# Kernel tuning notes

Hardware: AMD Instinct MI355X
Metric: run time of the kernel (lower is better)

## Reference

```python
import jax, jax.numpy as jnp
import numpy as np

I = 512   # input_size
H = 512   # hidden_size
Z = 0.1   # zoneout rate (eval-mode deterministic blend)
S = 128   # number of segments
B = 64    # batch


def setup_inputs() -> dict:
    rng = np.random.default_rng(0)
    durs = rng.integers(4, 13, size=(S, B)).astype(np.int64)  # [S, B], all >= 1
    T = int(durs.sum(0).max())
    key = jax.random.key(0)
    k0, k1, k2, k3, k4 = jax.random.split(key, 5)
    k = 1.0 / np.sqrt(H)
    x = jax.random.normal(k0, (T, B, I), jnp.float32)
    W_ih = jax.random.uniform(k1, (4 * H, I), jnp.float32, -k, k)
    W_hh = jax.random.uniform(k2, (4 * H, H), jnp.float32, -k, k)
    b_ih = jax.random.uniform(k3, (4 * H,), jnp.float32, -k, k)
    b_hh = jax.random.uniform(k4, (4 * H,), jnp.float32, -k, k)
    return {"x": x, "durs": jnp.asarray(durs), "W_ih": W_ih, "W_hh": W_hh,
            "b_ih": b_ih, "b_hh": b_hh}


def _duration_masks(durs, T):
    # durs: [S, B] -> per-batch segment-end (reset) frame indices and masks
    durs_bs = durs.T                                   # [B, S]
    reset_idx = jnp.cumsum(durs_bs, axis=1) - 1        # [B, S] last frame of each segment
    mel_lengths = jnp.sum(durs_bs, axis=1)             # [B]
    t = jnp.arange(T)
    reset_mask = jnp.any(t[None, :, None] == reset_idx[:, None, :], axis=-1)  # [B, T]
    valid = t[None, :] < mel_lengths[:, None]          # [B, T] frames within mel length
    retain = (~reset_mask) & valid                     # state kept where not reset/pad
    return reset_idx, retain.T, valid.T                # retain/valid as [T, B]


def reference(x, durs, W_ih, W_hh, b_ih, b_hh):
    T, Bb, _ = x.shape
    reset_idx, retain, valid = _duration_masks(durs, T)
    # Precompute the input contribution to the gates for all timesteps (one big GEMM)
    xg = jnp.einsum('tbi,gi->tbg', x, W_ih) + b_ih + b_hh   # [T, B, 4H]
    retain_f = retain.astype(x.dtype)                       # [T, B]

    def step(carry, inp):
        h, c = carry
        xg_t, retain_t = inp
        gates = xg_t + h @ W_hh.T                           # [B, 4H]
        i, f, g, o = jnp.split(gates, 4, axis=-1)           # torch LSTMCell order i,f,g,o
        i = jax.nn.sigmoid(i); f = jax.nn.sigmoid(f); o = jax.nn.sigmoid(o)
        g = jnp.tanh(g)
        c_new = f * c + i * g
        h_new = o * jnp.tanh(c_new)
        # eval-mode zoneout: deterministic blend with previous state
        h_z = Z * h + (1.0 - Z) * h_new
        c_z = Z * c + (1.0 - Z) * c_new
        m = retain_t[:, None]                               # zero state at segment resets / padding
        return (h_z * m, c_z * m), h_z

    h0 = jnp.zeros((Bb, H), x.dtype)
    (h, c), outputs = jax.lax.scan(step, (h0, h0), (xg, retain_f))
    outputs = outputs * valid[:, :, None].astype(outputs.dtype)  # [T, B, H]
    # segout: hidden state at each segment's last frame -> [B, S, H]
    segout = jnp.take_along_axis(outputs.transpose(1, 0, 2), reset_idx[:, :, None], axis=1)
    return outputs, h, c, segout
```

## Files before the change

### kernel.cpp

```cpp
#include <hip/hip_runtime.h>
#include <hip/hip_fp16.h>

#define IDIM 512
#define HDIM 512
#define NGATE 2048
#define SEGS 128
#define BATCH 64
#define ZK 0.1f

typedef _Float16 f16;
typedef _Float16 f16x8 __attribute__((ext_vector_type(8)));
typedef float f32x4 __attribute__((ext_vector_type(4)));

__device__ __forceinline__ void gload16(const void* g, void* l) {
  __builtin_amdgcn_global_load_lds((const __attribute__((address_space(1))) void*)g,
                                   (__attribute__((address_space(3))) void*)l, 16, 0, 0);
}
__device__ __forceinline__ float sigmoidf_(float x) { return 1.0f / (1.0f + __expf(-x)); }
__device__ __forceinline__ float tanhf_(float x) { return 2.0f / (1.0f + __expf(-2.0f * x)) - 1.0f; }

__global__ void prep_kernel(const int* __restrict__ durs, int4* __restrict__ meta,
                            int* __restrict__ Mk, int* __restrict__ mel) {
  __shared__ int hist[16];
  __shared__ int cur[16];
  int tid = threadIdx.x;
  if (tid < 16) hist[tid] = 0;
  __syncthreads();
  int b = tid;
  for (int s = 0; s < SEGS; ++s) atomicAdd(&hist[durs[s * BATCH + b] & 15], 1);
  __syncthreads();
  if (tid == 0) {
    int run = 0;
    for (int d = 15; d >= 0; --d) { cur[d] = run; run += hist[d]; }
    for (int kk = 0; kk < 12; ++kk) Mk[kk] = cur[kk];
  }
  __syncthreads();
  int run = 0;
  for (int s = 0; s < SEGS; ++s) {
    int d = durs[s * BATCH + b] & 15;
    int pos = atomicAdd(&cur[d], 1);
    meta[pos] = make_int4(run, b, s, d);
    run += d;
  }
  mel[b] = run;
}

__global__ void wprep_kernel(const float* __restrict__ Wih, const float* __restrict__ Whh,
                             const float* __restrict__ bih, const float* __restrict__ bhh,
                             f16* __restrict__ Wc, float* __restrict__ biasp) {
  int n = blockIdx.x;
  int G = n >> 6, q = (n >> 4) & 3, r = n & 15;
  int j = G * 16 + r;
  int orig = q * 512 + j;
  for (int kk = threadIdx.x; kk < 1024; kk += blockDim.x) {
    float v = (kk < 512) ? Wih[(size_t)orig * 512 + kk] : Whh[(size_t)orig * 512 + kk - 512];
    Wc[(size_t)n * 1024 + kk] = (f16)v;
  }
  if (threadIdx.x == 0) biasp[n] = bih[orig] + bhh[orig];
}

__global__ void xconv_kernel(const float* __restrict__ x, f16* __restrict__ xh, long n8) {
  long i = (long)blockIdx.x * blockDim.x + threadIdx.x;
  long stride = (long)gridDim.x * blockDim.x;
  for (; i < n8; i += stride) {
    const float4* p = (const float4*)(x + i * 8);
    float4 a = p[0], bv = p[1];
    f16x8 o;
    o[0] = (f16)a.x;  o[1] = (f16)a.y;  o[2] = (f16)a.z;  o[3] = (f16)a.w;
    o[4] = (f16)bv.x; o[5] = (f16)bv.y; o[6] = (f16)bv.z; o[7] = (f16)bv.w;
    *(f16x8*)(xh + i * 8) = o;
  }
}

__global__ void zero_kernel(float* __restrict__ out, const int* __restrict__ mel,
                            int T, int total) {
  int tb = T * BATCH;
  for (int bid = blockIdx.x; bid < total; bid += gridDim.x) {
    if (bid < tb) {
      int t = bid / BATCH, b = bid - t * BATCH;
      if (t < mel[b]) continue;
      float4* p = (float4*)(out + (size_t)bid * HDIM);
      p[threadIdx.x] = make_float4(0.f, 0.f, 0.f, 0.f);
    } else {
      int e = bid - tb;
      float4* p = (float4*)(out + (size_t)tb * HDIM + (size_t)e * HDIM);
      p[threadIdx.x] = make_float4(0.f, 0.f, 0.f, 0.f);
    }
  }
}

template <bool FIRST>
__global__ __launch_bounds__(512, 1)
void step256_kernel(const f16* __restrict__ xh, const f16* __restrict__ Wc,
                    const float* __restrict__ biasp,
                    const f16* __restrict__ hprev, f16* __restrict__ hnext,
                    float* __restrict__ cst,
                    const int4* __restrict__ meta, const int* __restrict__ Mk,
                    float* __restrict__ out, int T, int k) {
  const int mk = Mk[k];
  const int id = blockIdx.y * 8 + blockIdx.x;
  const int xcd = id & 7, slot = id >> 3;
  const int by = (slot & 3) * 8 + xcd;
  const int bx = slot >> 2;
  const int m0 = by * 256;
  if (m0 >= mk) return;
  const int n0 = bx * 256;

  __shared__ __align__(16) f16 As[2][256][64];
  __shared__ __align__(16) f16 Bs[2][256][64];
  __shared__ int4 metaS[256];

  const int tid = threadIdx.x;
  const int lane = tid & 63;
  const int w = tid >> 6;
  const int wr = w >> 2;
  const int wc = w & 3;
  const int lr = lane & 15;
  const int lk = lane >> 4;

  if (tid < 256) metaS[tid] = meta[m0 + tid];

  const int swzc = (((lane & 7) ^ ((lane >> 3) & 7)) << 3);
  size_t xoff[4];
  int ra4[4];
#pragma unroll
  for (int o = 0; o < 4; ++o) {
    int trow = o * 64 + w * 8 + (lane >> 3);
    int r = m0 + trow;
    int ra = (r < mk) ? r : 0;
    int4 mt = meta[ra];
    xoff[o] = ((size_t)(mt.x + k) * BATCH + mt.y) * IDIM + swzc;
    ra4[o] = ra;
  }

  auto stageA = [&](int o, int kb, int slot2) {
    const f16* src;
    if (FIRST || kb < 8) src = xh + xoff[o] + kb * 64;
    else src = hprev + (size_t)ra4[o] * HDIM + (kb - 8) * 64 + swzc;
    gload16(src, &As[slot2][o * 64 + w * 8][0]);
  };
  auto stageB = [&](int o, int kb, int slot2) {
    int trow = o * 64 + w * 8 + (lane >> 3);
    gload16(Wc + (size_t)(n0 + trow) * 1024 + (size_t)kb * 64 + swzc,
            &Bs[slot2][o * 64 + w * 8][0]);
  };

  auto lda = [&](int slot2, int h, int f, int ks) -> f16x8 {
    int row = wr * 128 + h * 64 + f * 16 + lr;
    int ch = (((ks * 4 + lk) ^ (lr & 7)) << 3);
    return *(const f16x8*)&As[slot2][row][ch];
  };
  auto ldb = [&](int slot2, int q, int ks) -> f16x8 {
    int row = wc * 64 + q * 16 + lr;
    int ch = (((ks * 4 + lk) ^ (lr & 7)) << 3);
    return *(const f16x8*)&Bs[slot2][row][ch];
  };

  f32x4 acc[8][4];
#pragma unroll
  for (int a = 0; a < 8; ++a)
#pragma unroll
    for (int bb = 0; bb < 4; ++bb) acc[a][bb] = (f32x4){0.f, 0.f, 0.f, 0.f};

  const int KB = FIRST ? 8 : 16;

#pragma unroll
  for (int o = 0; o < 4; ++o) stageA(o, 0, 0);
#pragma unroll
  for (int o = 0; o < 4; ++o) stageB(o, 0, 0);
#pragma unroll
  for (int o = 0; o < 4; ++o) stageA(o, 1, 1);
#pragma unroll
  for (int o = 0; o < 4; ++o) stageB(o, 1, 1);
  asm volatile("s_waitcnt vmcnt(8)" ::: "memory");
  __builtin_amdgcn_s_barrier();

  f16x8 aF[4][2], bF[4][2];

  for (int kt = 0; kt < KB; ++kt) {
    const int s = kt & 1;
    const bool st1 = (kt + 1 < KB);
    const bool st2 = (kt + 2 < KB);

#pragma unroll
    for (int f = 0; f < 4; ++f)
#pragma unroll
      for (int ks = 0; ks < 2; ++ks) aF[f][ks] = lda(s, 0, f, ks);
#pragma unroll
    for (int q = 0; q < 4; ++q)
#pragma unroll
      for (int ks = 0; ks < 2; ++ks) bF[q][ks] = ldb(s, q, ks);
    __builtin_amdgcn_s_barrier();
    __builtin_amdgcn_s_setprio(1);
#pragma unroll
    for (int f = 0; f < 4; ++f)
#pragma unroll
      for (int fn = 0; fn < 2; ++fn)
#pragma unroll
        for (int ks = 0; ks < 2; ++ks)
          acc[f][fn] = __builtin_amdgcn_mfma_f32_16x16x32_f16(aF[f][ks], bF[fn][ks], acc[f][fn], 0, 0, 0);
    __builtin_amdgcn_s_setprio(0);
    __builtin_amdgcn_s_barrier();

    if (st2) {
#pragma unroll
      for (int o = 0; o < 4; ++o) stageB(o, kt + 2, s);
    }
    __builtin_amdgcn_s_barrier();
    __builtin_amdgcn_s_setprio(1);
#pragma unroll
    for (int f = 0; f < 4; ++f)
#pragma unroll
      for (int fn = 2; fn < 4; ++fn)
#pragma unroll
        for (int ks = 0; ks < 2; ++ks)
          acc[f][fn] = __builtin_amdgcn_mfma_f32_16x16x32_f16(aF[f][ks], bF[fn][ks], acc[f][fn], 0, 0, 0);
    __builtin_amdgcn_s_setprio(0);
    __builtin_amdgcn_s_barrier();

#pragma unroll
    for (int f = 0; f < 4; ++f)
#pragma unroll
      for (int ks = 0; ks < 2; ++ks) aF[f][ks] = lda(s, 1, f, ks);
    if (st2) { stageA(0, kt + 2, s); stageA(2, kt + 2, s); }
    __builtin_amdgcn_s_barrier();
    __builtin_amdgcn_s_setprio(1);
#pragma unroll
    for (int f = 0; f < 4; ++f)
#pragma unroll
      for (int fn = 0; fn < 2; ++fn)
#pragma unroll
        for (int ks = 0; ks < 2; ++ks)
          acc[4 + f][fn] = __builtin_amdgcn_mfma_f32_16x16x32_f16(aF[f][ks], bF[fn][ks], acc[4 + f][fn], 0, 0, 0);
    __builtin_amdgcn_s_setprio(0);
    __builtin_amdgcn_s_barrier();

    if (st2) { stageA(1, kt + 2, s); stageA(3, kt + 2, s); }
    __builtin_amdgcn_s_setprio(1);
#pragma unroll
    for (int f = 0; f < 4; ++f)
#pragma unroll
      for (int fn = 2; fn < 4; ++fn)
#pragma unroll
        for (int ks = 0; ks < 2; ++ks)
          acc[4 + f][fn] = __builtin_amdgcn_mfma_f32_16x16x32_f16(aF[f][ks], bF[fn][ks], acc[4 + f][fn], 0, 0, 0);
    __builtin_amdgcn_s_setprio(0);
    if (st2) {
      asm volatile("s_waitcnt vmcnt(8)" ::: "memory");
    } else if (st1) {
      asm volatile("s_waitcnt vmcnt(0)" ::: "memory");
    }
    __builtin_amdgcn_s_barrier();
  }

  float bq[4];
#pragma unroll
  for (int q = 0; q < 4; ++q) bq[q] = biasp[n0 + wc * 64 + q * 16 + lr];
  const int j = ((n0 + wc * 64) >> 6) * 16 + lr;
  const size_t segoff = (size_t)T * BATCH * HDIM + (size_t)2 * BATCH * HDIM;

#pragma unroll
  for (int fm = 0; fm < 8; ++fm) {
#pragma unroll
    for (int reg = 0; reg < 4; ++reg) {
      int m = m0 + wr * 128 + fm * 16 + ((lane >> 4) << 2) + reg;
      if (m >= mk) continue;
      int4 mt = metaS[m - m0];
      float gi = acc[fm][0][reg] + bq[0];
      float gf = acc[fm][1][reg] + bq[1];
      float gg = acc[fm][2][reg] + bq[2];
      float go = acc[fm][3][reg] + bq[3];
      float iv = sigmoidf_(gi), fv = sigmoidf_(gf);
      float gv = tanhf_(gg), ov = sigmoidf_(go);
      float cp, hp;
      if (FIRST) { cp = 0.f; hp = 0.f; }
      else {
        cp = cst[(size_t)m * HDIM + j];
        hp = (float)hprev[(size_t)m * HDIM + j];
      }
      float cn = fv * cp + iv * gv;
      float hn = ov * tanhf_(cn);
      float hz = ZK * hp + (1.f - ZK) * hn;
      float cz = ZK * cp + (1.f - ZK) * cn;
      out[((size_t)(mt.x + k) * BATCH + mt.y) * HDIM + j] = hz;
      if (k == mt.w - 1) {
        out[segoff + ((size_t)mt.y * SEGS + mt.z) * HDIM + j] = hz;
      } else {
        hnext[(size_t)m * HDIM + j] = (f16)hz;
        cst[(size_t)m * HDIM + j] = cz;
      }
    }
  }
}

template <bool FIRST>
__global__ void step_kernel(const f16* __restrict__ xh, const f16* __restrict__ Wc,
                            const float* __restrict__ biasp,
                            const f16* __restrict__ hprev, f16* __restrict__ hnext,
                            float* __restrict__ cst,
                            const int4* __restrict__ meta, const int* __restrict__ Mk,
                            float* __restrict__ out, int T, int k) {
  const int mk = Mk[k];
  const int id = blockIdx.y * 16 + blockIdx.x;
  const int xcd = id & 7, slot = id >> 3;
  const int by = (slot & 7) * 8 + xcd;
  const int bx = slot >> 3;
  const int m0 = by * 128;
  if (m0 >= mk) return;
  const int n0 = bx * 128;

  __shared__ __align__(16) f16 At[128][64];
  __shared__ __align__(16) f16 Bt[128][64];
  __shared__ int4 metaS[128];

  const int tid = threadIdx.x;
  const int lane = tid & 63;
  const int w = tid >> 6;
  const int wr = w >> 1, wc = w & 1;

  if (tid < 128) metaS[tid] = meta[m0 + tid];

  const f16* xsrc[4];
  const f16* hsrc[4];
  const f16* wsrc[4];
#pragma unroll
  for (int i = 0; i < 4; ++i) {
    int r = m0 + w * 32 + i * 8 + (lane >> 3);
    int ra = (r < mk) ? r : 0;
    int4 mt = meta[ra];
    xsrc[i] = xh + ((size_t)(mt.x + k) * BATCH + mt.y) * IDIM;
    hsrc[i] = hprev + (size_t)ra * HDIM;
    wsrc[i] = Wc + (size_t)(n0 + w * 32 + i * 8 + (lane >> 3)) * 1024;
  }
  const int koff = (lane & 7) * 8;

  f32x4 acc[4][4];
#pragma unroll
  for (int a = 0; a < 4; ++a)
#pragma unroll
    for (int bb = 0; bb < 4; ++bb) acc[a][bb] = (f32x4){0.f, 0.f, 0.f, 0.f};

  const int KB = FIRST ? 8 : 16;
  for (int kb = 0; kb < KB; ++kb) {
    __syncthreads();
#pragma unroll
    for (int i = 0; i < 4; ++i) {
      const f16* s;
      if (FIRST) s = xsrc[i] + kb * 64 + koff;
      else       s = (kb < 8) ? (xsrc[i] + kb * 64 + koff) : (hsrc[i] + (kb - 8) * 64 + koff);
      gload16(s, &At[w * 32 + i * 8][0]);
    }
#pragma unroll
    for (int i = 0; i < 4; ++i) gload16(wsrc[i] + kb * 64 + koff, &Bt[w * 32 + i * 8][0]);
    __syncthreads();

    const int lr = lane & 15;
    const int lk = (lane >> 4) * 8;
#pragma unroll
    for (int ks = 0; ks < 2; ++ks) {
      f16x8 af[4], bfr[4];
#pragma unroll
      for (int f = 0; f < 4; ++f) af[f] = *(const f16x8*)&At[wr * 64 + f * 16 + lr][ks * 32 + lk];
#pragma unroll
      for (int f = 0; f < 4; ++f) bfr[f] = *(const f16x8*)&Bt[wc * 64 + f * 16 + lr][ks * 32 + lk];
#pragma unroll
      for (int fm = 0; fm < 4; ++fm)
#pragma unroll
        for (int fn = 0; fn < 4; ++fn)
          acc[fm][fn] = __builtin_amdgcn_mfma_f32_16x16x32_f16(af[fm], bfr[fn], acc[fm][fn], 0, 0, 0);
    }
  }

  const int r15 = lane & 15;
  float bq[4];
#pragma unroll
  for (int q = 0; q < 4; ++q) bq[q] = biasp[n0 + wc * 64 + q * 16 + r15];
  const int j = ((n0 + wc * 64) >> 6) * 16 + r15;
  const size_t segoff = (size_t)T * BATCH * HDIM + (size_t)2 * BATCH * HDIM;

#pragma unroll
  for (int fm = 0; fm < 4; ++fm) {
#pragma unroll
    for (int reg = 0; reg < 4; ++reg) {
      int m = m0 + wr * 64 + fm * 16 + ((lane >> 4) << 2) + reg;
      if (m >= mk) continue;
      int4 mt = metaS[m - m0];
      float gi = acc[fm][0][reg] + bq[0];
      float gf = acc[fm][1][reg] + bq[1];
      float gg = acc[fm][2][reg] + bq[2];
      float go = acc[fm][3][reg] + bq[3];
      float iv = sigmoidf_(gi), fv = sigmoidf_(gf);
      float gv = tanhf_(gg), ov = sigmoidf_(go);
      float cp, hp;
      if (FIRST) { cp = 0.f; hp = 0.f; }
      else {
        cp = cst[(size_t)m * HDIM + j];
        hp = (float)hprev[(size_t)m * HDIM + j];
      }
      float cn = fv * cp + iv * gv;
      float hn = ov * tanhf_(cn);
      float hz = ZK * hp + (1.f - ZK) * hn;
      float cz = ZK * cp + (1.f - ZK) * cn;
      out[((size_t)(mt.x + k) * BATCH + mt.y) * HDIM + j] = hz;
      if (k == mt.w - 1) {
        out[segoff + ((size_t)mt.y * SEGS + mt.z) * HDIM + j] = hz;
      } else {
        hnext[(size_t)m * HDIM + j] = (f16)hz;
        cst[(size_t)m * HDIM + j] = cz;
      }
    }
  }
}

extern "C" void kernel_launch(void* const* d_in, const int* in_sizes, int n_in,
                              void* d_out, int out_size, void* d_ws, size_t ws_size,
                              hipStream_t stream) {
  const float* x = (const float*)d_in[0];
  const int* durs = (const int*)d_in[1];
  const float* Wih = (const float*)d_in[2];
  const float* Whh = (const float*)d_in[3];
  const float* bih = (const float*)d_in[4];
  const float* bhh = (const float*)d_in[5];
  float* out = (float*)d_out;
  const int T = in_sizes[0] / (BATCH * IDIM);

  char* ws = (char*)d_ws;
  size_t off = 0;
  auto alloc = [&](size_t bytes) {
    void* p = ws + off;
    off = (off + bytes + 255) & ~(size_t)255;
    return p;
  };
  f16* xh     = (f16*)alloc((size_t)T * BATCH * IDIM * 2);
  f16* Wc     = (f16*)alloc((size_t)NGATE * 1024 * 2);
  float* biasp= (float*)alloc((size_t)NGATE * 4);
  f16* hst0   = (f16*)alloc((size_t)SEGS * BATCH * HDIM * 2);
  f16* hst1   = (f16*)alloc((size_t)SEGS * BATCH * HDIM * 2);
  float* cst  = (float*)alloc((size_t)SEGS * BATCH * HDIM * 4);
  int4* meta  = (int4*)alloc((size_t)SEGS * BATCH * 16);
  int* Mk     = (int*)alloc(64);
  int* mel    = (int*)alloc(64);

  prep_kernel<<<1, 64, 0, stream>>>(durs, meta, Mk, mel);
  wprep_kernel<<<NGATE, 256, 0, stream>>>(Wih, Whh, bih, bhh, Wc, biasp);
  long n8 = (long)T * BATCH * IDIM / 8;
  xconv_kernel<<<2048, 256, 0, stream>>>(x, xh, n8);
  zero_kernel<<<2048, 128, 0, stream>>>(out, mel, T, T * BATCH + 128);

  dim3 hgrid(8, 32);
  step256_kernel<true><<<hgrid, 512, 0, stream>>>(xh, Wc, biasp, hst0, hst1, cst, meta, Mk, out, T, 0);
  for (int k = 1; k < 8; ++k) {
    f16* hp = (k & 1) ? hst1 : hst0;
    f16* hn = (k & 1) ? hst0 : hst1;
    step256_kernel<false><<<hgrid, 512, 0, stream>>>(xh, Wc, biasp, hp, hn, cst, meta, Mk, out, T, k);
  }
  dim3 sgrid(16, 64);
  for (int k = 8; k < 12; ++k) {
    f16* hp = (k & 1) ? hst1 : hst0;
    f16* hn = (k & 1) ? hst0 : hst1;
    step_kernel<false><<<sgrid, 256, 0, stream>>>(xh, Wc, biasp, hp, hn, cst, meta, Mk, out, T, k);
  }
}
```

Before: 725.7 us.

## Rework 256x256 step GEMM to 4 waves with 128x128 per-wave tiles

The large-tile step kernel drops from 8 waves (512 threads) to 4 waves (256 threads), and each wave now computes a 128x128 output tile with a 64-entry accumulator array instead of 128x64. The k-loop is simplified to two MFMA phases per k-tile with fewer barriers, and all next-tile loads are issued in one group. The block-to-tile mapping swizzle is changed, and the smaller step kernel loses its XCD-aware remap in favour of direct blockIdx mapping. Larger per-wave tiles improve fragment reuse and cut barrier overhead, but they raise register pressure and leave fewer waves to hide latency.

```diff
diff --git a/kernel.cpp b/kernel.cpp
--- a/kernel.cpp
+++ b/kernel.cpp
@@ -90,7 +90,7 @@
 }
 
 template <bool FIRST>
-__global__ __launch_bounds__(512, 1)
+__global__ __launch_bounds__(256, 1)
 void step256_kernel(const f16* __restrict__ xh, const f16* __restrict__ Wc,
                     const float* __restrict__ biasp,
                     const f16* __restrict__ hprev, f16* __restrict__ hnext,
@@ -99,9 +99,8 @@
                     float* __restrict__ out, int T, int k) {
   const int mk = Mk[k];
   const int id = blockIdx.y * 8 + blockIdx.x;
-  const int xcd = id & 7, slot = id >> 3;
-  const int by = (slot & 3) * 8 + xcd;
-  const int bx = slot >> 2;
+  const int swz = (id & 7) * 32 + (id >> 3);
+  const int by = swz >> 3, bx = swz & 7;
   const int m0 = by * 256;
   if (m0 >= mk) return;
   const int n0 = bx * 256;
@@ -113,181 +112,163 @@
   const int tid = threadIdx.x;
   const int lane = tid & 63;
   const int w = tid >> 6;
-  const int wr = w >> 2;
-  const int wc = w & 3;
+  const int wr = w >> 1;
+  const int wc = w & 1;
   const int lr = lane & 15;
   const int lk = lane >> 4;
 
-  if (tid < 256) metaS[tid] = meta[m0 + tid];
+  metaS[tid] = meta[m0 + tid];
 
   const int swzc = (((lane & 7) ^ ((lane >> 3) & 7)) << 3);
-  size_t xoff[4];
-  int ra4[4];
-#pragma unroll
-  for (int o = 0; o < 4; ++o) {
-    int trow = o * 64 + w * 8 + (lane >> 3);
+  unsigned xoff[8];
+  int ra8[8];
+#pragma unroll
+  for (int o = 0; o < 8; ++o) {
+    int trow = o * 32 + w * 8 + (lane >> 3);
     int r = m0 + trow;
     int ra = (r < mk) ? r : 0;
     int4 mt = meta[ra];
-    xoff[o] = ((size_t)(mt.x + k) * BATCH + mt.y) * IDIM + swzc;
-    ra4[o] = ra;
-  }
-
-  auto stageA = [&](int o, int kb, int slot2) {
+    xoff[o] = (unsigned)(((mt.x + k) * BATCH + mt.y) * IDIM + swzc);
+    ra8[o] = ra;
+  }
+
+  auto stageA = [&](int o, int kb, int slot) {
     const f16* src;
-    if (FIRST || kb < 8) src = xh + xoff[o] + kb * 64;
-    else src = hprev + (size_t)ra4[o] * HDIM + (kb - 8) * 64 + swzc;
-    gload16(src, &As[slot2][o * 64 + w * 8][0]);
+    if (FIRST || kb < 8) src = xh + (size_t)xoff[o] + kb * 64;
+    else src = hprev + (size_t)ra8[o] * HDIM + (kb - 8) * 64 + swzc;
+    gload16(src, &As[slot][o * 32 + w * 8][0]);
   };
-  auto stageB = [&](int o, int kb, int slot2) {
-    int trow = o * 64 + w * 8 + (lane >> 3);
+  auto stageB = [&](int o, int kb, int slot) {
+    int trow = o * 32 + w * 8 + (lane >> 3);
     gload16(Wc + (size_t)(n0 + trow) * 1024 + (size_t)kb * 64 + swzc,
-            &Bs[slot2][o * 64 + w * 8][0]);
+            &Bs[slot][o * 32 + w * 8][0]);
   };
 
-  auto lda = [&](int slot2, int h, int f, int ks) -> f16x8 {
-    int row = wr * 128 + h * 64 + f * 16 + lr;
+  auto lda = [&](int slot, int mf, int ks) -> f16x8 {
+    int row = wr * 128 + mf * 16 + lr;
     int ch = (((ks * 4 + lk) ^ (lr & 7)) << 3);
-    return *(const f16x8*)&As[slot2][row][ch];
+    return *(const f16x8*)&As[slot][row][ch];
   };
-  auto ldb = [&](int slot2, int q, int ks) -> f16x8 {
-    int row = wc * 64 + q * 16 + lr;
+  auto ldb = [&](int slot, int nf, int ks) -> f16x8 {
+    int row = wc * 128 + nf * 16 + lr;
     int ch = (((ks * 4 + lk) ^ (lr & 7)) << 3);
-    return *(const f16x8*)&Bs[slot2][row][ch];
+    return *(const f16x8*)&Bs[slot][row][ch];
   };
 
-  f32x4 acc[8][4];
+  f32x4 acc[8][8];
 #pragma unroll
   for (int a = 0; a < 8; ++a)
 #pragma unroll
-    for (int bb = 0; bb < 4; ++bb) acc[a][bb] = (f32x4){0.f, 0.f, 0.f, 0.f};
+    for (int bb = 0; bb < 8; ++bb) acc[a][bb] = (f32x4){0.f, 0.f, 0.f, 0.f};
 
   const int KB = FIRST ? 8 : 16;
 
 #pragma unroll
-  for (int o = 0; o < 4; ++o) stageA(o, 0, 0);
-#pragma unroll
-  for (int o = 0; o < 4; ++o) stageB(o, 0, 0);
-#pragma unroll
-  for (int o = 0; o < 4; ++o) stageA(o, 1, 1);
-#pragma unroll
-  for (int o = 0; o < 4; ++o) stageB(o, 1, 1);
-  asm volatile("s_waitcnt vmcnt(8)" ::: "memory");
+  for (int o = 0; o < 8; ++o) { stageA(o, 0, 0); }
+#pragma unroll
+  for (int o = 0; o < 8; ++o) { stageB(o, 0, 0); }
+#pragma unroll
+  for (int o = 0; o < 8; ++o) { stageA(o, 1, 1); }
+#pragma unroll
+  for (int o = 0; o < 8; ++o) { stageB(o, 1, 1); }
+  asm volatile("s_waitcnt vmcnt(16)" ::: "memory");
   __builtin_amdgcn_s_barrier();
-
-  f16x8 aF[4][2], bF[4][2];
 
   for (int kt = 0; kt < KB; ++kt) {
     const int s = kt & 1;
     const bool st1 = (kt + 1 < KB);
     const bool st2 = (kt + 2 < KB);
 
-#pragma unroll
-    for (int f = 0; f < 4; ++f)
-#pragma unroll
-      for (int ks = 0; ks < 2; ++ks) aF[f][ks] = lda(s, 0, f, ks);
-#pragma unroll
-    for (int q = 0; q < 4; ++q)
-#pragma unroll
-      for (int ks = 0; ks < 2; ++ks) bF[q][ks] = ldb(s, q, ks);
+    f16x8 bF[8][2], aF0[8], aF1[8];
+#pragma unroll
+    for (int nf = 0; nf < 8; ++nf) {
+      bF[nf][0] = ldb(s, nf, 0);
+      bF[nf][1] = ldb(s, nf, 1);
+    }
+#pragma unroll
+    for (int mf = 0; mf < 8; ++mf) aF0[mf] = lda(s, mf, 0);
+
+    __builtin_amdgcn_s_setprio(1);
+#pragma unroll
+    for (int mf = 0; mf < 8; ++mf)
+#pragma unroll
+      for (int nf = 0; nf < 8; ++nf)
+        acc[mf][nf] = __builtin_amdgcn_mfma_f32_16x16x32_f16(aF0[mf], bF[nf][0], acc[mf][nf], 0, 0, 0);
+    __builtin_amdgcn_s_setprio(0);
+
+#pragma unroll
+    for (int mf = 0; mf < 8; ++mf) aF1[mf] = lda(s, mf, 1);
+
     __builtin_amdgcn_s_barrier();
+
+    if (st2) {
+#pragma unroll
+      for (int o = 0; o < 8; ++o) { stageA(o, kt + 2, s); }
+#pragma unroll
+      for (int o = 0; o < 8; ++o) { stageB(o, kt + 2, s); }
+    }
+
     __builtin_amdgcn_s_setprio(1);
 #pragma unroll
-    for (int f = 0; f < 4; ++f)
-#pragma unroll
-      for (int fn = 0; fn < 2; ++fn)
-#pragma unroll
-        for (int ks = 0; ks < 2; ++ks)
-          acc[f][fn] = __builtin_amdgcn_mfma_f32_16x16x32_f16(aF[f][ks], bF[fn][ks], acc[f][fn], 0, 0, 0);
+    for (int mf = 0; mf < 8; ++mf)
+#pragma unroll
+      for (int nf = 0; nf < 8; ++nf)
+        acc[mf][nf] = __builtin_amdgcn_mfma_f32_16x16x32_f16(aF1[mf], bF[nf][1], acc[mf][nf], 0, 0, 0);
     __builtin_amdgcn_s_setprio(0);
-    __builtin_amdgcn_s_barrier();
 
     if (st2) {
-#pragma unroll
-      for (int o = 0; o < 4; ++o) stageB(o, kt + 2, s);
-    }
-    __builtin_amdgcn_s_barrier();
-    __builtin_amdgcn_s_setprio(1);
-#pragma unroll
-    for (int f = 0; f < 4; ++f)
-#pragma unroll
-      for (int fn = 2; fn < 4; ++fn)
-#pragma unroll
-        for (int ks = 0; ks < 2; ++ks)
-          acc[f][fn] = __builtin_amdgcn_mfma_f32_16x16x32_f16(aF[f][ks], bF[fn][ks], acc[f][fn], 0, 0, 0);
-    __builtin_amdgcn_s_setprio(0);
-    __builtin_amdgcn_s_barrier();
-
-#pragma unroll
-    for (int f = 0; f < 4; ++f)
-#pragma unroll
-      for (int ks = 0; ks < 2; ++ks) aF[f][ks] = lda(s, 1, f, ks);
-    if (st2) { stageA(0, kt + 2, s); stageA(2, kt + 2, s); }
-    __builtin_amdgcn_s_barrier();
-    __builtin_amdgcn_s_setprio(1);
-#pragma unroll
-    for (int f = 0; f < 4; ++f)
-#pragma unroll
-      for (int fn = 0; fn < 2; ++fn)
-#pragma unroll
-        for (int ks = 0; ks < 2; ++ks)
-          acc[4 + f][fn] = __builtin_amdgcn_mfma_f32_16x16x32_f16(aF[f][ks], bF[fn][ks], acc[4 + f][fn], 0, 0, 0);
-    __builtin_amdgcn_s_setprio(0);
-    __builtin_amdgcn_s_barrier();
-
-    if (st2) { stageA(1, kt + 2, s); stageA(3, kt + 2, s); }
-    __builtin_amdgcn_s_setprio(1);
-#pragma unroll
-    for (int f = 0; f < 4; ++f)
-#pragma unroll
-      for (int fn = 2; fn < 4; ++fn)
-#pragma unroll
-        for (int ks = 0; ks < 2; ++ks)
-          acc[4 + f][fn] = __builtin_amdgcn_mfma_f32_16x16x32_f16(aF[f][ks], bF[fn][ks], acc[4 + f][fn], 0, 0, 0);
-    __builtin_amdgcn_s_setprio(0);
-    if (st2) {
-      asm volatile("s_waitcnt vmcnt(8)" ::: "memory");
+      asm volatile("s_waitcnt vmcnt(16)" ::: "memory");
     } else if (st1) {
       asm volatile("s_waitcnt vmcnt(0)" ::: "memory");
     }
     __builtin_amdgcn_s_barrier();
   }
 
-  float bq[4];
-#pragma unroll
-  for (int q = 0; q < 4; ++q) bq[q] = biasp[n0 + wc * 64 + q * 16 + lr];
-  const int j = ((n0 + wc * 64) >> 6) * 16 + lr;
+  float bq[2][4];
+#pragma unroll
+  for (int g2 = 0; g2 < 2; ++g2)
+#pragma unroll
+    for (int q = 0; q < 4; ++q)
+      bq[g2][q] = biasp[n0 + wc * 128 + g2 * 64 + q * 16 + lr];
+  int jg[2];
+#pragma unroll
+  for (int g2 = 0; g2 < 2; ++g2)
+    jg[g2] = ((n0 + wc * 128 + g2 * 64) >> 6) * 16 + lr;
   const size_t segoff = (size_t)T * BATCH * HDIM + (size_t)2 * BATCH * HDIM;
 
 #pragma unroll
-  for (int fm = 0; fm < 8; ++fm) {
+  for (int mf = 0; mf < 8; ++mf) {
 #pragma unroll
     for (int reg = 0; reg < 4; ++reg) {
-      int m = m0 + wr * 128 + fm * 16 + ((lane >> 4) << 2) + reg;
+      int m = m0 + wr * 128 + mf * 16 + ((lane >> 4) << 2) + reg;
       if (m >= mk) continue;
       int4 mt = metaS[m - m0];
-      float gi = acc[fm][0][reg] + bq[0];
-      float gf = acc[fm][1][reg] + bq[1];
-      float gg = acc[fm][2][reg] + bq[2];
-      float go = acc[fm][3][reg] + bq[3];
-      float iv = sigmoidf_(gi), fv = sigmoidf_(gf);
-      float gv = tanhf_(gg), ov = sigmoidf_(go);
-      float cp, hp;
-      if (FIRST) { cp = 0.f; hp = 0.f; }
-      else {
-        cp = cst[(size_t)m * HDIM + j];
-        hp = (float)hprev[(size_t)m * HDIM + j];
-      }
-      float cn = fv * cp + iv * gv;
-      float hn = ov * tanhf_(cn);
-      float hz = ZK * hp + (1.f - ZK) * hn;
-      float cz = ZK * cp + (1.f - ZK) * cn;
-      out[((size_t)(mt.x + k) * BATCH + mt.y) * HDIM + j] = hz;
-      if (k == mt.w - 1) {
-        out[segoff + ((size_t)mt.y * SEGS + mt.z) * HDIM + j] = hz;
-      } else {
-        hnext[(size_t)m * HDIM + j] = (f16)hz;
-        cst[(size_t)m * HDIM + j] = cz;
+#pragma unroll
+      for (int g2 = 0; g2 < 2; ++g2) {
+        int j = jg[g2];
+        float gi = acc[mf][g2 * 4 + 0][reg] + bq[g2][0];
+        float gf = acc[mf][g2 * 4 + 1][reg] + bq[g2][1];
+        float gg = acc[mf][g2 * 4 + 2][reg] + bq[g2][2];
+        float go = acc[mf][g2 * 4 + 3][reg] + bq[g2][3];
+        float iv = sigmoidf_(gi), fv = sigmoidf_(gf);
+        float gv = tanhf_(gg), ov = sigmoidf_(go);
+        float cp, hp;
+        if (FIRST) { cp = 0.f; hp = 0.f; }
+        else {
+          cp = cst[(size_t)m * HDIM + j];
+          hp = (float)hprev[(size_t)m * HDIM + j];
+        }
+        float cn = fv * cp + iv * gv;
+        float hn = ov * tanhf_(cn);
+        float hz = ZK * hp + (1.f - ZK) * hn;
+        float cz = ZK * cp + (1.f - ZK) * cn;
+        out[((size_t)(mt.x + k) * BATCH + mt.y) * HDIM + j] = hz;
+        if (k == mt.w - 1) {
+          out[segoff + ((size_t)mt.y * SEGS + mt.z) * HDIM + j] = hz;
+        } else {
+          hnext[(size_t)m * HDIM + j] = (f16)hz;
+          cst[(size_t)m * HDIM + j] = cz;
+        }
       }
     }
   }
@@ -301,13 +282,9 @@
                             const int4* __restrict__ meta, const int* __restrict__ Mk,
                             float* __restrict__ out, int T, int k) {
   const int mk = Mk[k];
-  const int id = blockIdx.y * 16 + blockIdx.x;
-  const int xcd = id & 7, slot = id >> 3;
-  const int by = (slot & 7) * 8 + xcd;
-  const int bx = slot >> 3;
-  const int m0 = by * 128;
+  const int m0 = blockIdx.y * 128;
   if (m0 >= mk) return;
-  const int n0 = bx * 128;
+  const int n0 = blockIdx.x * 128;
 
   __shared__ __align__(16) f16 At[128][64];
   __shared__ __align__(16) f16 Bt[128][64];
@@ -448,11 +425,11 @@
   zero_kernel<<<2048, 128, 0, stream>>>(out, mel, T, T * BATCH + 128);
 
   dim3 hgrid(8, 32);
-  step256_kernel<true><<<hgrid, 512, 0, stream>>>(xh, Wc, biasp, hst0, hst1, cst, meta, Mk, out, T, 0);
+  step256_kernel<true><<<hgrid, 256, 0, stream>>>(xh, Wc, biasp, hst0, hst1, cst, meta, Mk, out, T, 0);
   for (int k = 1; k < 8; ++k) {
     f16* hp = (k & 1) ? hst1 : hst0;
     f16* hn = (k & 1) ? hst0 : hst1;
-    step256_kernel<false><<<hgrid, 512, 0, stream>>>(xh, Wc, biasp, hp, hn, cst, meta, Mk, out, T, k);
+    step256_kernel<false><<<hgrid, 256, 0, stream>>>(xh, Wc, biasp, hp, hn, cst, meta, Mk, out, T, k);
   }
   dim3 sgrid(16, 64);
   for (int k = 8; k < 12; ++k) {
```

After: 693.9 us. -4.4%, faster.
